# Performance work log

Measured on AMD Instinct MI355X. Metric: run time of the kernel, lower is better.

The kernel has to match this reference:

```python
import jax, jax.numpy as jnp
import numpy as np

CONF_THRES = 0.2   # from __init__ default
IOU_THRES = 0.6    # from __init__ default
MAX_WH = 4096.0    # class-offset for multi-class NMS (yolov7 convention)
TOPK = 2048        # pre-NMS candidates per image
MAX_DET = 300      # max detections per image (yolov7 default)
B, N, NC = 8, 25200, 80


def setup_inputs() -> dict:
    key = jax.random.key(0)
    k1, k2, k3 = jax.random.split(key, 3)
    # decoded predictions: [cx, cy, w, h, obj, cls_0..cls_79]
    xywh = jax.random.uniform(k1, (B, N, 4)) * jnp.array([640.0, 640.0, 120.0, 120.0])
    obj = jax.random.uniform(k2, (B, N, 1))
    cls = jax.random.uniform(k3, (B, N, NC))
    preds = jnp.concatenate([xywh, obj, cls], axis=-1)  # [B, N, 85]
    return {"preds": preds}


def _xywh2xyxy(xywh):
    cx, cy, w, h = xywh[..., 0], xywh[..., 1], xywh[..., 2], xywh[..., 3]
    return jnp.stack([cx - w * 0.5, cy - h * 0.5, cx + w * 0.5, cy + h * 0.5], axis=-1)


def _box_iou(a, b):
    # a: [K,4], b: [K,4] -> [K,K] pairwise IoU
    area_a = (a[:, 2] - a[:, 0]) * (a[:, 3] - a[:, 1])
    area_b = (b[:, 2] - b[:, 0]) * (b[:, 3] - b[:, 1])
    lt = jnp.maximum(a[:, None, :2], b[None, :, :2])  # [K,K,2]
    rb = jnp.minimum(a[:, None, 2:], b[None, :, 2:])
    wh = jnp.clip(rb - lt, 0.0)
    inter = wh[..., 0] * wh[..., 1]
    return inter / (area_a[:, None] + area_b[None, :] - inter + 1e-9)


def _nms_single(pred):
    # pred: [N, 5+NC]
    boxes = _xywh2xyxy(pred[:, :4])                 # [N,4]
    scores_all = pred[:, 5:] * pred[:, 4:5]         # obj * cls  [N,NC]
    conf = jnp.max(scores_all, axis=-1)             # best-class conf
    cls_id = jnp.argmax(scores_all, axis=-1)
    scores = jnp.where(conf > CONF_THRES, conf, 0.0)

    # pre-NMS top-k candidates (sorted descending)
    top_scores, idx = jax.lax.top_k(scores, TOPK)
    top_boxes = boxes[idx]                          # [K,4]
    top_cls = cls_id[idx]                           # [K]
    top_valid = top_scores > CONF_THRES

    # per-class NMS via class offset so cross-class boxes never overlap
    offset_boxes = top_boxes + (top_cls.astype(top_boxes.dtype) * MAX_WH)[:, None]
    iou = _box_iou(offset_boxes, offset_boxes)      # [K,K]

    # greedy NMS over score-sorted candidates
    def body(i, state):
        keep, suppressed = state
        k_i = top_valid[i] & jnp.logical_not(suppressed[i])
        keep = keep.at[i].set(k_i)
        sup_new = suppressed | (k_i & (iou[i] > IOU_THRES))
        sup_new = sup_new.at[i].set(suppressed[i])  # never self-suppress
        return keep, sup_new

    keep, _ = jax.lax.fori_loop(
        0, TOPK, body,
        (jnp.zeros(TOPK, dtype=bool), jnp.zeros(TOPK, dtype=bool)))

    # take top MAX_DET kept detections
    keep_scores = jnp.where(keep, top_scores, -1.0)
    det_scores, det_idx = jax.lax.top_k(keep_scores, MAX_DET)
    det = jnp.concatenate(
        [top_boxes[det_idx],
         det_scores[:, None],
         top_cls[det_idx].astype(pred.dtype)[:, None]], axis=-1)  # [MAX_DET,6]
    det = jnp.where((det_scores > 0.0)[:, None], det, 0.0)
    return det


def reference(preds):
    # preds: [B, N, 5+NC] -> [B, MAX_DET, 6] (x1,y1,x2,y2,conf,cls), zero-padded
    return jax.vmap(_nms_single)(preds)
```

## Files before the change

### kernel.cpp

```cpp
#include <hip/hip_runtime.h>

#define BATCH 8
#define NPRED 25200
#define NCLS 80
#define ROWW 85
#define TOPKK 2048
#define MAXDET 300
#define CANDMAX 4096
#define NBUCKET 4096
#define CONF_T 0.2f
#define IOU_T 0.6f
#define CLS_OFF 4096.0f

#define MASKN 384
#define MCH (MASKN / 64)
#define MW 13

typedef unsigned long long u64;
typedef unsigned int u32;

__device__ __forceinline__ int bucket_of_key(u64 k) {
    float sc = __uint_as_float((u32)(k >> 32));
    int bkt = (int)(sc * (float)NBUCKET);
    return (bkt > NBUCKET - 1) ? (NBUCKET - 1) : bkt;
}

__global__ __launch_bounds__(256) void k_score(
    const float* __restrict__ preds,
    u64* __restrict__ keys,
    unsigned char* __restrict__ cls8)
{
    __shared__ float rows[64 * ROWW];
    const int t = threadIdx.x;
    const size_t rowbase = (size_t)blockIdx.x * 64;

    const float4* src = reinterpret_cast<const float4*>(preds + rowbase * ROWW);
    float4* dst = reinterpret_cast<float4*>(rows);
    #pragma unroll
    for (int i = t; i < 64 * ROWW / 4; i += 256) dst[i] = src[i];
    __syncthreads();

    const int r = t >> 2;
    const int j = t & 3;
    const float* p = rows + r * ROWW;
    const float obj = p[4];

    float best = -1.0f;
    int bi = 0;
    #pragma unroll
    for (int tt = 0; tt < 20; ++tt) {
        int c = j + 4 * tt;
        float s = __fmul_rn(obj, p[5 + c]);
        if (s > best) { best = s; bi = c; }
    }
    #pragma unroll
    for (int d = 1; d <= 2; d <<= 1) {
        float os = __shfl_xor(best, d);
        int oi = __shfl_xor(bi, d);
        if (os > best || (os == best && oi < bi)) { best = os; bi = oi; }
    }

    if (j == 0) {
        unsigned gid = (unsigned)rowbase + r;
        u64 key = 0ull;
        if (best > CONF_T) {
            key = ((u64)__float_as_uint(best) << 32) | (0xFFFFFFFFu - (gid % NPRED));
        }
        keys[gid] = key;
        cls8[gid] = (unsigned char)bi;
    }
}

__global__ __launch_bounds__(1024) void k_scan(
    const u64* __restrict__ keys,
    u32* __restrict__ hist_g,
    u32* __restrict__ bstart_g,
    u32* __restrict__ balloc_g,
    int* __restrict__ tb_g,
    u32* __restrict__ stored_g)
{
    __shared__ u32 histL[NBUCKET];
    __shared__ u32 wtot[16];
    __shared__ u32 wsuf[16];
    __shared__ int s_tb;
    __shared__ u32 s_stored;

    const int b = blockIdx.x;
    const int t = threadIdx.x;
    const int lane = t & 63;
    const int wave = t >> 6;
    const u64* bk = keys + (size_t)b * NPRED;

    for (int i = t; i < NBUCKET; i += 1024) histL[i] = 0u;
    __syncthreads();

    for (int i = t; i < NPRED; i += 1024) {
        u64 k = bk[i];
        if (k) atomicAdd(&histL[bucket_of_key(k)], 1u);
    }
    __syncthreads();

    u32 h0 = histL[4 * t], h1 = histL[4 * t + 1], h2 = histL[4 * t + 2], h3 = histL[4 * t + 3];
    u32 ps = h0 + h1 + h2 + h3;

    u32 v = ps;
    #pragma unroll
    for (int off = 1; off < 64; off <<= 1) {
        u32 u2 = __shfl_down(v, off);
        if (lane + off < 64) v += u2;
    }
    if (lane == 0) wtot[wave] = v;
    __syncthreads();
    if (t < 16) {
        u32 w = wtot[t];
        u32 s = w;
        #pragma unroll
        for (int off = 1; off < 16; off <<= 1) {
            u32 u2 = __shfl_down(s, off);
            if (t + off < 16) s += u2;
        }
        wsuf[t] = s - w;
    }
    __syncthreads();
    u32 suffix_t = v + wsuf[wave];
    u32 snext = suffix_t - ps;

    u32 b3 = snext;
    u32 b2 = b3 + h3;
    u32 b1 = b2 + h2;
    u32 b0 = b1 + h1;
    const size_t B0 = (size_t)b * NBUCKET;
    hist_g[B0 + 4 * t + 0] = h0;
    hist_g[B0 + 4 * t + 1] = h1;
    hist_g[B0 + 4 * t + 2] = h2;
    hist_g[B0 + 4 * t + 3] = h3;
    bstart_g[B0 + 4 * t + 0] = b0;
    bstart_g[B0 + 4 * t + 1] = b1;
    bstart_g[B0 + 4 * t + 2] = b2;
    bstart_g[B0 + 4 * t + 3] = b3;
    balloc_g[B0 + 4 * t + 0] = b0;
    balloc_g[B0 + 4 * t + 1] = b1;
    balloc_g[B0 + 4 * t + 2] = b2;
    balloc_g[B0 + 4 * t + 3] = b3;

    if (t == 0) {
        s_tb = 0;
        s_stored = (suffix_t < (u32)CANDMAX) ? suffix_t : (u32)CANDMAX;
    }
    __syncthreads();
    {
        u32 c3 = b3 + h3, c2 = b2 + h2, c1 = b1 + h1, c0 = b0 + h0;
        if (c3 >= TOPKK && b3 < TOPKK) { s_tb = 4 * t + 3; s_stored = (c3 < (u32)CANDMAX) ? c3 : (u32)CANDMAX; }
        if (c2 >= TOPKK && b2 < TOPKK) { s_tb = 4 * t + 2; s_stored = (c2 < (u32)CANDMAX) ? c2 : (u32)CANDMAX; }
        if (c1 >= TOPKK && b1 < TOPKK) { s_tb = 4 * t + 1; s_stored = (c1 < (u32)CANDMAX) ? c1 : (u32)CANDMAX; }
        if (c0 >= TOPKK && b0 < TOPKK) { s_tb = 4 * t + 0; s_stored = (c0 < (u32)CANDMAX) ? c0 : (u32)CANDMAX; }
    }
    __syncthreads();
    if (t == 0) { tb_g[b] = s_tb; stored_g[b] = s_stored; }
}

__global__ __launch_bounds__(256) void k_compact(
    const u64* __restrict__ keys,
    u32* __restrict__ balloc_g,
    const int* __restrict__ tb_g,
    u64* __restrict__ cand_g)
{
    unsigned gid = blockIdx.x * 256 + threadIdx.x;
    if (gid >= BATCH * NPRED) return;
    u64 k = keys[gid];
    if (!k) return;
    int b = gid / NPRED;
    int bkt = bucket_of_key(k);
    if (bkt < tb_g[b]) return;
    u32 slot = atomicAdd(&balloc_g[(size_t)b * NBUCKET + bkt], 1u);
    if (slot < CANDMAX) cand_g[(size_t)b * CANDMAX + slot] = k;
}

struct RankPhase {
    u32 histL[NBUCKET];
    u32 bstartL[NBUCKET];
};
struct NmsPhase {
    u32 masks32[MASKN * MW];
    float4 cbx[MASKN];
    float carea[MASKN];
    float4 kb[MAXDET];
};

__global__ __launch_bounds__(1024) void k_finish(
    const float* __restrict__ preds,
    const unsigned char* __restrict__ cls8,
    const u32* __restrict__ hist_g,
    const u32* __restrict__ bstart_g,
    const int* __restrict__ tb_g,
    const u32* __restrict__ stored_g,
    const u64* __restrict__ cand_g,
    float* __restrict__ out)
{
    __shared__ union { RankPhase rk; NmsPhase nms; } u;
    __shared__ u64 candL[CANDMAX];
    __shared__ unsigned short rank2cand[TOPKK];
    __shared__ float4 sbox[MASKN];
    __shared__ float sscore[MASKN];
    __shared__ float scls[MASKN];
    __shared__ u64 validw[MCH];

    const int b = blockIdx.x;
    const int t = threadIdx.x;
    const int lane = t & 63;
    const int wave = t >> 6;
    float* ob = out + (size_t)b * MAXDET * 6;
    const u32 stored = stored_g[b];
    const int tb = tb_g[b];

    for (int i = tb + t; i < NBUCKET; i += 1024) {
        u.rk.histL[i] = hist_g[(size_t)b * NBUCKET + i];
        u.rk.bstartL[i] = bstart_g[(size_t)b * NBUCKET + i];
    }
    for (int i = t; i < TOPKK; i += 1024) rank2cand[i] = 0xFFFFu;
    for (int i = t; i < CANDMAX; i += 1024)
        if ((u32)i < stored) candL[i] = cand_g[(size_t)b * CANDMAX + i];
    if (t < MASKN) {
        sbox[t] = make_float4(0.f, 0.f, 0.f, 0.f);
        sscore[t] = 0.f;
        scls[t] = 0.f;
    }
    __syncthreads();

    for (u32 i = t; i < stored; i += 1024) {
        u64 k = candL[i];
        int bkt = bucket_of_key(k);
        u32 base = u.rk.bstartL[bkt];
        u32 end = base + u.rk.histL[bkt];
        if (end > stored) end = stored;
        u32 r = base;
        for (u32 jx = base; jx < end; ++jx) r += (candL[jx] > k) ? 1u : 0u;
        if (r < TOPKK) rank2cand[r] = (unsigned short)i;
        if (r < MASKN) {
            float sc = __uint_as_float((u32)(k >> 32));
            unsigned idx = 0xFFFFFFFFu - (u32)(k & 0xFFFFFFFFu);
            const float* p = preds + ((size_t)b * NPRED + idx) * ROWW;
            float cx = p[0], cy = p[1], w = p[2], h = p[3];
            float hw = __fmul_rn(w, 0.5f);
            float hh = __fmul_rn(h, 0.5f);
            sbox[r] = make_float4(__fsub_rn(cx, hw), __fsub_rn(cy, hh),
                                  __fadd_rn(cx, hw), __fadd_rn(cy, hh));
            sscore[r] = sc;
            scls[r] = (float)cls8[(size_t)b * NPRED + idx];
        }
    }
    __syncthreads();

    if (t < MASKN) {
        float sc = sscore[t];
        float cl = scls[t];
        float4 bb = sbox[t];
        float off = __fmul_rn(cl, CLS_OFF);
        float4 obx = make_float4(__fadd_rn(bb.x, off), __fadd_rn(bb.y, off),
                                 __fadd_rn(bb.z, off), __fadd_rn(bb.w, off));
        u.nms.cbx[t] = obx;
        u.nms.carea[t] = __fmul_rn(__fsub_rn(obx.z, obx.x), __fsub_rn(obx.w, obx.y));
        u64 vb = __ballot(sc > CONF_T);
        if (lane == 0) validw[wave] = vb;
    }
    __syncthreads();

    for (int tu = 0; tu < 3; ++tu) {
        int uidx = wave + 16 * tu;
        if (uidx >= 42) break;
        int q, s;
        if (uidx < 12)      { q = 0; s = uidx; }
        else if (uidx < 22) { q = 1; s = uidx - 12 + 2; }
        else if (uidx < 30) { q = 2; s = uidx - 22 + 4; }
        else if (uidx < 36) { q = 3; s = uidx - 30 + 6; }
        else if (uidx < 40) { q = 4; s = uidx - 36 + 8; }
        else                { q = 5; s = uidx - 40 + 10; }

        const int r = q * 64 + lane;
        const float4 me = u.nms.cbx[r];
        const float aA = u.nms.carea[r];
        const int j0 = s * 32;
        u32 acc = 0u;
        #pragma unroll 8
        for (int jj = 0; jj < 32; ++jj) {
            const int jx = j0 + jj;
            float4 cb = u.nms.cbx[jx];
            float lx = fmaxf(me.x, cb.x), ly = fmaxf(me.y, cb.y);
            float rx = fminf(me.z, cb.z), ry = fminf(me.w, cb.w);
            float iw = fmaxf(__fsub_rn(rx, lx), 0.0f);
            float ih = fmaxf(__fsub_rn(ry, ly), 0.0f);
            float inter = __fmul_rn(iw, ih);
            float denom = __fadd_rn(__fsub_rn(__fadd_rn(aA, u.nms.carea[jx]), inter), 1e-9f);
            bool sv = inter > __fmul_rn(IOU_T, denom);
            acc |= ((u32)sv) << jj;
        }
        if (s == 2 * q || s == 2 * q + 1) {
            int shift = r - j0;
            u32 dm = (shift < 0) ? ~0u : ((shift >= 31) ? 0u : (~0u << (shift + 1)));
            acc &= dm;
        }
        u.nms.masks32[r * MW + s] = acc;
    }
    __syncthreads();
    if (wave != 0) return;

    const u64 below = (lane == 0) ? 0ull : (~0ull >> (64 - lane));
    u64 S[MCH];
    #pragma unroll
    for (int w = 0; w < MCH; ++w) S[w] = 0ull;
    int nk = 0;
    bool done = false, allfull = true;

    #pragma unroll
    for (int c = 0; c < MCH; ++c) {
        if (done) break;
        u64 vw = validw[c];
        u64 eligible = vw & ~S[c];
        const int rbase = (c * 64 + lane) * MW;
        u64 Mu = ((u64)u.nms.masks32[rbase + 2 * c + 1] << 32) |
                 (u64)u.nms.masks32[rbase + 2 * c];
        bool elig = (eligible >> lane) & 1ull;
        if (eligible) {
            int cap = MAXDET - nk;
            u64 edge = __ballot(elig && ((Mu & eligible) != 0ull));
            u64 keptm;
            if (edge == 0ull) {
                int rank = __popcll(eligible & below);
                keptm = __ballot(elig && (rank < cap));
            } else {
                u64 km = 0ull, supm = 0ull;
                int cnt = 0;
                for (int m = 0; m < 64 && cnt < cap; ++m) {
                    if (!((eligible >> m) & 1ull)) continue;
                    if ((supm >> m) & 1ull) continue;
                    km |= 1ull << m;
                    ++cnt;
                    supm |= __shfl(Mu, m);
                }
                keptm = km;
            }
            if ((keptm >> lane) & 1ull) {
                int pos = nk + __popcll(keptm & below);
                int i = c * 64 + lane;
                float4 bb = sbox[i];
                u.nms.kb[pos] = u.nms.cbx[i];
                float* row = ob + pos * 6;
                row[0] = bb.x; row[1] = bb.y; row[2] = bb.z; row[3] = bb.w;
                row[4] = sscore[i]; row[5] = scls[i];
            }
            nk += __popcll(keptm);
            if (nk >= MAXDET) {
                done = true;
            } else if (keptm) {
                for (int w = c + 1; w < MCH; ++w) {
                    u64 v = ((keptm >> lane) & 1ull)
                        ? (((u64)u.nms.masks32[rbase + 2 * w + 1] << 32) |
                           (u64)u.nms.masks32[rbase + 2 * w])
                        : 0ull;
                    v |= __shfl_xor(v, 1);  v |= __shfl_xor(v, 2);
                    v |= __shfl_xor(v, 4);  v |= __shfl_xor(v, 8);
                    v |= __shfl_xor(v, 16); v |= __shfl_xor(v, 32);
                    S[w] |= v;
                }
            }
        }
        if (vw != ~0ull) { allfull = false; break; }
    }

    if (!done && allfull && nk < MAXDET) {
        __threadfence_block();
        for (int c = MCH; c < TOPKK / 64; ++c) {
            int r = c * 64 + lane;
            unsigned short ci = rank2cand[r];
            bool valid = (ci != 0xFFFFu);
            u64 validmask = __ballot(valid);
            if (validmask == 0ull) break;

            float sc = 0.f, cl = 0.f;
            float bx1 = 0.f, by1 = 0.f, bx2 = 0.f, by2 = 0.f;
            if (valid) {
                u64 k = candL[ci];
                sc = __uint_as_float((u32)(k >> 32));
                unsigned idx = 0xFFFFFFFFu - (u32)(k & 0xFFFFFFFFu);
                const float* p = preds + ((size_t)b * NPRED + idx) * ROWW;
                float cx = p[0], cy = p[1], w = p[2], h = p[3];
                float hw = __fmul_rn(w, 0.5f);
                float hh = __fmul_rn(h, 0.5f);
                bx1 = __fsub_rn(cx, hw); by1 = __fsub_rn(cy, hh);
                bx2 = __fadd_rn(cx, hw); by2 = __fadd_rn(cy, hh);
                cl = (float)cls8[(size_t)b * NPRED + idx];
            }
            float off = __fmul_rn(cl, CLS_OFF);
            float x1 = __fadd_rn(bx1, off), y1 = __fadd_rn(by1, off);
            float x2 = __fadd_rn(bx2, off), y2 = __fadd_rn(by2, off);
            float areaA = __fmul_rn(__fsub_rn(x2, x1), __fsub_rn(y2, y1));

            bool sup = false;
            for (int jx = 0; jx < nk; ++jx) {
                float4 k4 = u.nms.kb[jx];
                float lx = fmaxf(x1, k4.x), ly = fmaxf(y1, k4.y);
                float rx = fminf(x2, k4.z), ry = fminf(y2, k4.w);
                float iw = fmaxf(__fsub_rn(rx, lx), 0.0f);
                float ih = fmaxf(__fsub_rn(ry, ly), 0.0f);
                float inter = __fmul_rn(iw, ih);
                float areaB = __fmul_rn(__fsub_rn(k4.z, k4.x), __fsub_rn(k4.w, k4.y));
                float denom = __fadd_rn(__fsub_rn(__fadd_rn(areaA, areaB), inter), 1e-9f);
                if (inter > __fmul_rn(IOU_T, denom)) sup = true;
            }
            u64 supprev = __ballot(sup);

            u32 sb_lo = 0u, sb_hi = 0u;
            for (int m = 0; m < 64; ++m) {
                float mx1 = __shfl(x1, m), my1 = __shfl(y1, m);
                float mx2 = __shfl(x2, m), my2 = __shfl(y2, m);
                float lx = fmaxf(x1, mx1), ly = fmaxf(y1, my1);
                float rx = fminf(x2, mx2), ry = fminf(y2, my2);
                float iw = fmaxf(__fsub_rn(rx, lx), 0.0f);
                float ih = fmaxf(__fsub_rn(ry, ly), 0.0f);
                float inter = __fmul_rn(iw, ih);
                float areaB = __fmul_rn(__fsub_rn(mx2, mx1), __fsub_rn(my2, my1));
                float denom = __fadd_rn(__fsub_rn(__fadd_rn(areaA, areaB), inter), 1e-9f);
                bool s = (m != lane) && (inter > __fmul_rn(IOU_T, denom));
                if (m < 32) sb_lo |= ((u32)s) << m;
                else        sb_hi |= ((u32)s) << (m - 32);
            }

            u64 eligible = validmask & ~supprev;
            u64 mysb = (((u64)sb_hi << 32) | (u64)sb_lo);
            bool iselig = (eligible >> lane) & 1ull;
            u64 edgeball = __ballot(iselig && ((mysb & eligible & below) != 0ull));

            u64 keptm;
            int cap = MAXDET - nk;
            if (edgeball == 0ull) {
                int rank = __popcll(eligible & below);
                keptm = __ballot(iselig && (rank < cap));
            } else {
                u64 km = 0ull;
                int cnt = 0;
                for (int m = 0; m < 64 && cnt < cap; ++m) {
                    if (!((validmask >> m) & 1ull)) break;
                    if ((supprev >> m) & 1ull) continue;
                    u32 mlo = (u32)__shfl((int)sb_lo, m);
                    u32 mhi = (u32)__shfl((int)sb_hi, m);
                    u64 supby = (((u64)mhi << 32) | (u64)mlo);
                    if (supby & km) continue;
                    km |= 1ull << m;
                    ++cnt;
                }
                keptm = km;
            }

            if ((keptm >> lane) & 1ull) {
                int pos = nk + __popcll(keptm & below);
                u.nms.kb[pos] = make_float4(x1, y1, x2, y2);
                float* row = ob + pos * 6;
                row[0] = bx1; row[1] = by1; row[2] = bx2; row[3] = by2;
                row[4] = sc;  row[5] = cl;
            }
            __threadfence_block();
            nk += __popcll(keptm);
            if (nk >= MAXDET) break;
            if (validmask != ~0ull) break;
        }
    }

    for (int x = nk * 6 + lane; x < MAXDET * 6; x += 64) ob[x] = 0.0f;
}

extern "C" void kernel_launch(void* const* d_in, const int* in_sizes, int n_in,
                              void* d_out, int out_size, void* d_ws, size_t ws_size,
                              hipStream_t stream) {
    const float* preds = (const float*)d_in[0];
    float* out = (float*)d_out;

    u32* hist_g   = (u32*)d_ws;
    u32* bstart_g = hist_g + BATCH * NBUCKET;
    u32* balloc_g = bstart_g + BATCH * NBUCKET;
    int* tb_g     = (int*)(balloc_g + BATCH * NBUCKET);
    u32* stored_g = (u32*)(tb_g + 8);
    u64* keys     = (u64*)(stored_g + 8);
    unsigned char* cls8 = (unsigned char*)(keys + BATCH * NPRED);
    u64* cand_g   = (u64*)(cls8 + BATCH * NPRED);

    hipLaunchKernelGGL(k_score, dim3(BATCH * NPRED / 64), dim3(256), 0, stream,
                       preds, keys, cls8);
    hipLaunchKernelGGL(k_scan, dim3(BATCH), dim3(1024), 0, stream,
                       keys, hist_g, bstart_g, balloc_g, tb_g, stored_g);
    hipLaunchKernelGGL(k_compact, dim3((BATCH * NPRED + 255) / 256), dim3(256), 0, stream,
                       keys, balloc_g, tb_g, cand_g);
    hipLaunchKernelGGL(k_finish, dim3(BATCH), dim3(1024), 0, stream,
                       preds, cls8, hist_g, bstart_g, tb_g, stored_g, cand_g, out);
}
```

Baseline: 67.29 us.

## Fuse scan, compact and finish kernels into one per-image kernel with LDS tables

Merges the histogram/scan, candidate compaction and rank/NMS kernels into a single per-batch block. Bucket tables and candidates stay in shared memory instead of making a round trip through global workspace, which removes two launches and their global traffic. In exchange, compaction now runs on only 8 blocks, each re-reading its image's 25200 keys, instead of on a wide grid. The score kernel also switches its row staging to direct global-to-LDS loads.

```diff
diff --git a/kernel.cpp b/kernel.cpp
--- a/kernel.cpp
+++ b/kernel.cpp
@@ -30,16 +30,23 @@
     u64* __restrict__ keys,
     unsigned char* __restrict__ cls8)
 {
-    __shared__ float rows[64 * ROWW];
+    __shared__ float4 rows4[64 * ROWW / 4 + 4];
     const int t = threadIdx.x;
+    const int lane = t & 63;
+    const int wave = t >> 6;
     const size_t rowbase = (size_t)blockIdx.x * 64;
-
     const float4* src = reinterpret_cast<const float4*>(preds + rowbase * ROWW);
-    float4* dst = reinterpret_cast<float4*>(rows);
-    #pragma unroll
-    for (int i = t; i < 64 * ROWW / 4; i += 256) dst[i] = src[i];
-    __syncthreads();
-
+
+    for (int q = wave; q < 21; q += 4) {
+        __builtin_amdgcn_global_load_lds(
+            (const __attribute__((address_space(1))) void*)(src + q * 64 + lane),
+            (__attribute__((address_space(3))) void*)(rows4 + q * 64),
+            16, 0, 0);
+    }
+    if (t < 16) rows4[1344 + t] = src[1344 + t];
+    __syncthreads();
+
+    const float* rows = reinterpret_cast<const float*>(rows4);
     const int r = t >> 2;
     const int j = t & 3;
     const float* p = rows + r * ROWW;
@@ -71,15 +78,31 @@
     }
 }
 
-__global__ __launch_bounds__(1024) void k_scan(
+struct Tables {
+    u32 histL[NBUCKET];
+    u32 bstartL[NBUCKET];
+    u32 ballocL[NBUCKET];
+};
+struct NmsP {
+    u32 masks32[MASKN * MW];
+    float4 cbx[MASKN];
+    float carea[MASKN];
+    float4 kb[MAXDET];
+};
+
+__global__ __launch_bounds__(1024) void k_main(
+    const float* __restrict__ preds,
+    const unsigned char* __restrict__ cls8,
     const u64* __restrict__ keys,
-    u32* __restrict__ hist_g,
-    u32* __restrict__ bstart_g,
-    u32* __restrict__ balloc_g,
-    int* __restrict__ tb_g,
-    u32* __restrict__ stored_g)
+    float* __restrict__ out)
 {
-    __shared__ u32 histL[NBUCKET];
+    __shared__ union { Tables tb; NmsP nms; } u;
+    __shared__ u64 candL[CANDMAX];
+    __shared__ unsigned short rank2cand[TOPKK];
+    __shared__ float4 sbox[MASKN];
+    __shared__ float sscore[MASKN];
+    __shared__ float scls[MASKN];
+    __shared__ u64 validw[MCH];
     __shared__ u32 wtot[16];
     __shared__ u32 wsuf[16];
     __shared__ int s_tb;
@@ -90,19 +113,19 @@
     const int lane = t & 63;
     const int wave = t >> 6;
     const u64* bk = keys + (size_t)b * NPRED;
-
-    for (int i = t; i < NBUCKET; i += 1024) histL[i] = 0u;
-    __syncthreads();
-
+    float* ob = out + (size_t)b * MAXDET * 6;
+
+    for (int i = t; i < NBUCKET; i += 1024) u.tb.histL[i] = 0u;
+    __syncthreads();
     for (int i = t; i < NPRED; i += 1024) {
         u64 k = bk[i];
-        if (k) atomicAdd(&histL[bucket_of_key(k)], 1u);
-    }
-    __syncthreads();
-
-    u32 h0 = histL[4 * t], h1 = histL[4 * t + 1], h2 = histL[4 * t + 2], h3 = histL[4 * t + 3];
+        if (k) atomicAdd(&u.tb.histL[bucket_of_key(k)], 1u);
+    }
+    __syncthreads();
+
+    u32 h0 = u.tb.histL[4 * t], h1 = u.tb.histL[4 * t + 1];
+    u32 h2 = u.tb.histL[4 * t + 2], h3 = u.tb.histL[4 * t + 3];
     u32 ps = h0 + h1 + h2 + h3;
-
     u32 v = ps;
     #pragma unroll
     for (int off = 1; off < 64; off <<= 1) {
@@ -121,6 +144,7 @@
         }
         wsuf[t] = s - w;
     }
+    if (t == 0) s_tb = 0;
     __syncthreads();
     u32 suffix_t = v + wsuf[wave];
     u32 snext = suffix_t - ps;
@@ -129,24 +153,15 @@
     u32 b2 = b3 + h3;
     u32 b1 = b2 + h2;
     u32 b0 = b1 + h1;
-    const size_t B0 = (size_t)b * NBUCKET;
-    hist_g[B0 + 4 * t + 0] = h0;
-    hist_g[B0 + 4 * t + 1] = h1;
-    hist_g[B0 + 4 * t + 2] = h2;
-    hist_g[B0 + 4 * t + 3] = h3;
-    bstart_g[B0 + 4 * t + 0] = b0;
-    bstart_g[B0 + 4 * t + 1] = b1;
-    bstart_g[B0 + 4 * t + 2] = b2;
-    bstart_g[B0 + 4 * t + 3] = b3;
-    balloc_g[B0 + 4 * t + 0] = b0;
-    balloc_g[B0 + 4 * t + 1] = b1;
-    balloc_g[B0 + 4 * t + 2] = b2;
-    balloc_g[B0 + 4 * t + 3] = b3;
-
-    if (t == 0) {
-        s_tb = 0;
-        s_stored = (suffix_t < (u32)CANDMAX) ? suffix_t : (u32)CANDMAX;
-    }
+    u.tb.bstartL[4 * t + 0] = b0;
+    u.tb.bstartL[4 * t + 1] = b1;
+    u.tb.bstartL[4 * t + 2] = b2;
+    u.tb.bstartL[4 * t + 3] = b3;
+    u.tb.ballocL[4 * t + 0] = b0;
+    u.tb.ballocL[4 * t + 1] = b1;
+    u.tb.ballocL[4 * t + 2] = b2;
+    u.tb.ballocL[4 * t + 3] = b3;
+    if (t == 0) s_stored = (suffix_t < (u32)CANDMAX) ? suffix_t : (u32)CANDMAX;
     __syncthreads();
     {
         u32 c3 = b3 + h3, c2 = b2 + h2, c1 = b1 + h1, c0 = b0 + h0;
@@ -156,82 +171,32 @@
         if (c0 >= TOPKK && b0 < TOPKK) { s_tb = 4 * t + 0; s_stored = (c0 < (u32)CANDMAX) ? c0 : (u32)CANDMAX; }
     }
     __syncthreads();
-    if (t == 0) { tb_g[b] = s_tb; stored_g[b] = s_stored; }
-}
-
-__global__ __launch_bounds__(256) void k_compact(
-    const u64* __restrict__ keys,
-    u32* __restrict__ balloc_g,
-    const int* __restrict__ tb_g,
-    u64* __restrict__ cand_g)
-{
-    unsigned gid = blockIdx.x * 256 + threadIdx.x;
-    if (gid >= BATCH * NPRED) return;
-    u64 k = keys[gid];
-    if (!k) return;
-    int b = gid / NPRED;
-    int bkt = bucket_of_key(k);
-    if (bkt < tb_g[b]) return;
-    u32 slot = atomicAdd(&balloc_g[(size_t)b * NBUCKET + bkt], 1u);
-    if (slot < CANDMAX) cand_g[(size_t)b * CANDMAX + slot] = k;
-}
-
-struct RankPhase {
-    u32 histL[NBUCKET];
-    u32 bstartL[NBUCKET];
-};
-struct NmsPhase {
-    u32 masks32[MASKN * MW];
-    float4 cbx[MASKN];
-    float carea[MASKN];
-    float4 kb[MAXDET];
-};
-
-__global__ __launch_bounds__(1024) void k_finish(
-    const float* __restrict__ preds,
-    const unsigned char* __restrict__ cls8,
-    const u32* __restrict__ hist_g,
-    const u32* __restrict__ bstart_g,
-    const int* __restrict__ tb_g,
-    const u32* __restrict__ stored_g,
-    const u64* __restrict__ cand_g,
-    float* __restrict__ out)
-{
-    __shared__ union { RankPhase rk; NmsPhase nms; } u;
-    __shared__ u64 candL[CANDMAX];
-    __shared__ unsigned short rank2cand[TOPKK];
-    __shared__ float4 sbox[MASKN];
-    __shared__ float sscore[MASKN];
-    __shared__ float scls[MASKN];
-    __shared__ u64 validw[MCH];
-
-    const int b = blockIdx.x;
-    const int t = threadIdx.x;
-    const int lane = t & 63;
-    const int wave = t >> 6;
-    float* ob = out + (size_t)b * MAXDET * 6;
-    const u32 stored = stored_g[b];
-    const int tb = tb_g[b];
-
-    for (int i = tb + t; i < NBUCKET; i += 1024) {
-        u.rk.histL[i] = hist_g[(size_t)b * NBUCKET + i];
-        u.rk.bstartL[i] = bstart_g[(size_t)b * NBUCKET + i];
-    }
+    const int tb_ = s_tb;
+    const u32 stored = s_stored;
+
     for (int i = t; i < TOPKK; i += 1024) rank2cand[i] = 0xFFFFu;
-    for (int i = t; i < CANDMAX; i += 1024)
-        if ((u32)i < stored) candL[i] = cand_g[(size_t)b * CANDMAX + i];
     if (t < MASKN) {
         sbox[t] = make_float4(0.f, 0.f, 0.f, 0.f);
         sscore[t] = 0.f;
         scls[t] = 0.f;
     }
+    for (int i = t; i < NPRED; i += 1024) {
+        u64 k = bk[i];
+        if (k) {
+            int bkt = bucket_of_key(k);
+            if (bkt >= tb_) {
+                u32 pos = atomicAdd(&u.tb.ballocL[bkt], 1u);
+                if (pos < CANDMAX) candL[pos] = k;
+            }
+        }
+    }
     __syncthreads();
 
     for (u32 i = t; i < stored; i += 1024) {
         u64 k = candL[i];
         int bkt = bucket_of_key(k);
-        u32 base = u.rk.bstartL[bkt];
-        u32 end = base + u.rk.histL[bkt];
+        u32 base = u.tb.bstartL[bkt];
+        u32 end = base + u.tb.histL[bkt];
         if (end > stored) end = stored;
         u32 r = base;
         for (u32 jx = base; jx < end; ++jx) r += (candL[jx] > k) ? 1u : 0u;
@@ -353,14 +318,14 @@
                 done = true;
             } else if (keptm) {
                 for (int w = c + 1; w < MCH; ++w) {
-                    u64 v = ((keptm >> lane) & 1ull)
+                    u64 v2 = ((keptm >> lane) & 1ull)
                         ? (((u64)u.nms.masks32[rbase + 2 * w + 1] << 32) |
                            (u64)u.nms.masks32[rbase + 2 * w])
                         : 0ull;
-                    v |= __shfl_xor(v, 1);  v |= __shfl_xor(v, 2);
-                    v |= __shfl_xor(v, 4);  v |= __shfl_xor(v, 8);
-                    v |= __shfl_xor(v, 16); v |= __shfl_xor(v, 32);
-                    S[w] |= v;
+                    v2 |= __shfl_xor(v2, 1);  v2 |= __shfl_xor(v2, 2);
+                    v2 |= __shfl_xor(v2, 4);  v2 |= __shfl_xor(v2, 8);
+                    v2 |= __shfl_xor(v2, 16); v2 |= __shfl_xor(v2, 32);
+                    S[w] |= v2;
                 }
             }
         }
@@ -474,21 +439,11 @@
     const float* preds = (const float*)d_in[0];
     float* out = (float*)d_out;
 
-    u32* hist_g   = (u32*)d_ws;
-    u32* bstart_g = hist_g + BATCH * NBUCKET;
-    u32* balloc_g = bstart_g + BATCH * NBUCKET;
-    int* tb_g     = (int*)(balloc_g + BATCH * NBUCKET);
-    u32* stored_g = (u32*)(tb_g + 8);
-    u64* keys     = (u64*)(stored_g + 8);
+    u64* keys = (u64*)d_ws;
     unsigned char* cls8 = (unsigned char*)(keys + BATCH * NPRED);
-    u64* cand_g   = (u64*)(cls8 + BATCH * NPRED);
 
     hipLaunchKernelGGL(k_score, dim3(BATCH * NPRED / 64), dim3(256), 0, stream,
                        preds, keys, cls8);
-    hipLaunchKernelGGL(k_scan, dim3(BATCH), dim3(1024), 0, stream,
-                       keys, hist_g, bstart_g, balloc_g, tb_g, stored_g);
-    hipLaunchKernelGGL(k_compact, dim3((BATCH * NPRED + 255) / 256), dim3(256), 0, stream,
-                       keys, balloc_g, tb_g, cand_g);
-    hipLaunchKernelGGL(k_finish, dim3(BATCH), dim3(1024), 0, stream,
-                       preds, cls8, hist_g, bstart_g, tb_g, stored_g, cand_g, out);
+    hipLaunchKernelGGL(k_main, dim3(BATCH), dim3(1024), 0, stream,
+                       preds, cls8, keys, out);
 }
```

Result: faster. 64.09 us (-4.8%).

## Fuse score histogram into scoring kernel and load rows via global_load_lds

Applied to the files above, without the earlier changes.

Builds the per-image score-bucket histogram in k_score with global atomics, so k_scan no longer rereads all keys with only 8 blocks. The histogram is zeroed by a memset added before the launch. The row staging into shared memory now uses direct global-to-LDS loads instead of a register round trip. The cost is contended global atomics on hot buckets and one extra memset launch.

```diff
diff --git a/kernel.cpp b/kernel.cpp
--- a/kernel.cpp
+++ b/kernel.cpp
@@ -28,18 +28,26 @@
 __global__ __launch_bounds__(256) void k_score(
     const float* __restrict__ preds,
     u64* __restrict__ keys,
-    unsigned char* __restrict__ cls8)
+    unsigned char* __restrict__ cls8,
+    u32* __restrict__ hist_g)
 {
-    __shared__ float rows[64 * ROWW];
+    __shared__ float4 rows4[64 * ROWW / 4 + 4];
     const int t = threadIdx.x;
+    const int lane = t & 63;
+    const int wave = t >> 6;
     const size_t rowbase = (size_t)blockIdx.x * 64;
-
     const float4* src = reinterpret_cast<const float4*>(preds + rowbase * ROWW);
-    float4* dst = reinterpret_cast<float4*>(rows);
-    #pragma unroll
-    for (int i = t; i < 64 * ROWW / 4; i += 256) dst[i] = src[i];
-    __syncthreads();
-
+
+    for (int q = wave; q < 21; q += 4) {
+        __builtin_amdgcn_global_load_lds(
+            (const __attribute__((address_space(1))) void*)(src + q * 64 + lane),
+            (__attribute__((address_space(3))) void*)(rows4 + q * 64),
+            16, 0, 0);
+    }
+    if (t < 16) rows4[1344 + t] = src[1344 + t];
+    __syncthreads();
+
+    const float* rows = reinterpret_cast<const float*>(rows4);
     const int r = t >> 2;
     const int j = t & 3;
     const float* p = rows + r * ROWW;
@@ -68,18 +76,19 @@
         }
         keys[gid] = key;
         cls8[gid] = (unsigned char)bi;
+        if (key) {
+            atomicAdd(&hist_g[(gid / NPRED) * NBUCKET + bucket_of_key(key)], 1u);
+        }
     }
 }
 
 __global__ __launch_bounds__(1024) void k_scan(
-    const u64* __restrict__ keys,
-    u32* __restrict__ hist_g,
+    const u32* __restrict__ hist_g,
     u32* __restrict__ bstart_g,
     u32* __restrict__ balloc_g,
     int* __restrict__ tb_g,
     u32* __restrict__ stored_g)
 {
-    __shared__ u32 histL[NBUCKET];
     __shared__ u32 wtot[16];
     __shared__ u32 wsuf[16];
     __shared__ int s_tb;
@@ -89,18 +98,9 @@
     const int t = threadIdx.x;
     const int lane = t & 63;
     const int wave = t >> 6;
-    const u64* bk = keys + (size_t)b * NPRED;
-
-    for (int i = t; i < NBUCKET; i += 1024) histL[i] = 0u;
-    __syncthreads();
-
-    for (int i = t; i < NPRED; i += 1024) {
-        u64 k = bk[i];
-        if (k) atomicAdd(&histL[bucket_of_key(k)], 1u);
-    }
-    __syncthreads();
-
-    u32 h0 = histL[4 * t], h1 = histL[4 * t + 1], h2 = histL[4 * t + 2], h3 = histL[4 * t + 3];
+    const u32* H = hist_g + (size_t)b * NBUCKET;
+
+    u32 h0 = H[4 * t], h1 = H[4 * t + 1], h2 = H[4 * t + 2], h3 = H[4 * t + 3];
     u32 ps = h0 + h1 + h2 + h3;
 
     u32 v = ps;
@@ -121,6 +121,7 @@
         }
         wsuf[t] = s - w;
     }
+    if (t == 0) s_tb = 0;
     __syncthreads();
     u32 suffix_t = v + wsuf[wave];
     u32 snext = suffix_t - ps;
@@ -130,10 +131,6 @@
     u32 b1 = b2 + h2;
     u32 b0 = b1 + h1;
     const size_t B0 = (size_t)b * NBUCKET;
-    hist_g[B0 + 4 * t + 0] = h0;
-    hist_g[B0 + 4 * t + 1] = h1;
-    hist_g[B0 + 4 * t + 2] = h2;
-    hist_g[B0 + 4 * t + 3] = h3;
     bstart_g[B0 + 4 * t + 0] = b0;
     bstart_g[B0 + 4 * t + 1] = b1;
     bstart_g[B0 + 4 * t + 2] = b2;
@@ -143,10 +140,7 @@
     balloc_g[B0 + 4 * t + 2] = b2;
     balloc_g[B0 + 4 * t + 3] = b3;
 
-    if (t == 0) {
-        s_tb = 0;
-        s_stored = (suffix_t < (u32)CANDMAX) ? suffix_t : (u32)CANDMAX;
-    }
+    if (t == 0) s_stored = (suffix_t < (u32)CANDMAX) ? suffix_t : (u32)CANDMAX;
     __syncthreads();
     {
         u32 c3 = b3 + h3, c2 = b2 + h2, c1 = b1 + h1, c0 = b0 + h0;
@@ -353,14 +347,14 @@
                 done = true;
             } else if (keptm) {
                 for (int w = c + 1; w < MCH; ++w) {
-                    u64 v = ((keptm >> lane) & 1ull)
+                    u64 v2 = ((keptm >> lane) & 1ull)
                         ? (((u64)u.nms.masks32[rbase + 2 * w + 1] << 32) |
                            (u64)u.nms.masks32[rbase + 2 * w])
                         : 0ull;
-                    v |= __shfl_xor(v, 1);  v |= __shfl_xor(v, 2);
-                    v |= __shfl_xor(v, 4);  v |= __shfl_xor(v, 8);
-                    v |= __shfl_xor(v, 16); v |= __shfl_xor(v, 32);
-                    S[w] |= v;
+                    v2 |= __shfl_xor(v2, 1);  v2 |= __shfl_xor(v2, 2);
+                    v2 |= __shfl_xor(v2, 4);  v2 |= __shfl_xor(v2, 8);
+                    v2 |= __shfl_xor(v2, 16); v2 |= __shfl_xor(v2, 32);
+                    S[w] |= v2;
                 }
             }
         }
@@ -483,10 +477,12 @@
     unsigned char* cls8 = (unsigned char*)(keys + BATCH * NPRED);
     u64* cand_g   = (u64*)(cls8 + BATCH * NPRED);
 
+    hipMemsetAsync(hist_g, 0, (size_t)BATCH * NBUCKET * sizeof(u32), stream);
+
     hipLaunchKernelGGL(k_score, dim3(BATCH * NPRED / 64), dim3(256), 0, stream,
-                       preds, keys, cls8);
+                       preds, keys, cls8, hist_g);
     hipLaunchKernelGGL(k_scan, dim3(BATCH), dim3(1024), 0, stream,
-                       keys, hist_g, bstart_g, balloc_g, tb_g, stored_g);
+                       hist_g, bstart_g, balloc_g, tb_g, stored_g);
     hipLaunchKernelGGL(k_compact, dim3((BATCH * NPRED + 255) / 256), dim3(256), 0, stream,
                        keys, balloc_g, tb_g, cand_g);
     hipLaunchKernelGGL(k_finish, dim3(BATCH), dim3(1024), 0, stream,
```

After: 64.87 us. -3.6%, faster.
